# Kernel tuning notes

Measured on AMD Instinct MI355X. Metric: run time of the kernel, lower is better.

## Reference

```python
import jax, jax.numpy as jnp
import numpy as np

H = 64  # hidden size


def _lstm(hist, Wih, Whh, bih, bhh):
    # PyTorch single-layer LSTM, gate order [i, f, g, o]; hist: (T, in_dim)
    def step(carry, x):
        h, c = carry
        gates = Wih @ x + bih + Whh @ h + bhh  # (4H,)
        i, f, g, o = jnp.split(gates, 4)
        i, f, o = jax.nn.sigmoid(i), jax.nn.sigmoid(f), jax.nn.sigmoid(o)
        c = f * c + i * jnp.tanh(g)
        h = o * jnp.tanh(c)
        return (h, c), None
    h0 = jnp.zeros((H,), hist.dtype)
    (h, _), _ = jax.lax.scan(step, (h0, h0), hist)
    return h


def setup_inputs() -> dict:
    key = jax.random.key(0)
    ks = jax.random.split(key, 16)
    N, E, P, T = 100000, 3200000, 1000000, 200
    s = 0.05
    return {
        "node_feats": jax.random.normal(ks[0], (N, 2), jnp.float32),
        "edge_feats": jax.random.normal(ks[1], (E, 5), jnp.float32),
        "hist_tokens": jax.random.normal(ks[2], (T, 3), jnp.float32),
        "cand_pairs": jax.random.randint(ks[3], (P, 2), 0, N, jnp.int32),
        "N": N,
        "node_W": jax.random.normal(ks[4], (2, H), jnp.float32) * s,
        "node_b": jax.random.normal(ks[5], (H,), jnp.float32) * s,
        "edge_W": jax.random.normal(ks[6], (5, H), jnp.float32) * s,
        "edge_b": jax.random.normal(ks[7], (H,), jnp.float32) * s,
        "lstm_Wih": jax.random.normal(ks[8], (4 * H, 3), jnp.float32) * s,
        "lstm_Whh": jax.random.normal(ks[9], (4 * H, H), jnp.float32) * s,
        "lstm_bih": jax.random.normal(ks[10], (4 * H,), jnp.float32) * s,
        "lstm_bhh": jax.random.normal(ks[11], (4 * H,), jnp.float32) * s,
        "fuse_W1": jax.random.normal(ks[12], (3 * H + 2, H), jnp.float32) * s,
        "fuse_b1": jax.random.normal(ks[13], (H,), jnp.float32) * s,
        "fuse_W2": jax.random.normal(ks[14], (H, 1), jnp.float32) * s,
        "fuse_b2": jax.random.normal(ks[15], (1,), jnp.float32) * s,
    }


def reference(node_feats, edge_feats, hist_tokens, cand_pairs, N,
              node_W, node_b, edge_W, edge_b,
              lstm_Wih, lstm_Whh, lstm_bih, lstm_bhh,
              fuse_W1, fuse_b1, fuse_W2, fuse_b2):
    # encoder: mean-pooled node / edge MLPs -> (2H,)
    hn = jax.nn.relu(node_feats @ node_W + node_b).mean(0)
    he = jax.nn.relu(edge_feats @ edge_W + edge_b).mean(0)
    z_graph = jnp.concatenate([hn, he])  # (2H,)
    z_hist = _lstm(hist_tokens, lstm_Wih, lstm_Whh, lstm_bih, lstm_bhh)  # (H,)
    P = cand_pairs.shape[0]
    denom = jnp.float32(N - 1) + 1e-9
    cand = cand_pairs.astype(jnp.float32) / denom  # (P, 2)
    ctx = jnp.concatenate([z_graph, z_hist])  # (3H,)
    z = jnp.concatenate([jnp.broadcast_to(ctx, (P, 3 * H)), cand], axis=-1)  # (P, 3H+2)
    scores = jax.nn.relu(z @ fuse_W1 + fuse_b1) @ fuse_W2 + fuse_b2  # (P, 1)
    return scores[:, 0]
```

## Files before the change

kernel.cpp:

```cpp
#include <hip/hip_runtime.h>
#include <math.h>

#define H 64
#define WS_H 0
#define WS_FUSE 64
#define WS_CNT 320
#define WS_PART 384
#define LOG2E 1.4426950408889634f

__device__ __forceinline__ float fast_sigmoid(float x) {
    float e = exp2f(-LOG2E * x);
    return __builtin_amdgcn_rcpf(1.f + e);
}
__device__ __forceinline__ float fast_tanh(float x) {
    x = fminf(fmaxf(x, -9.f), 9.f);
    float e = exp2f((2.f * LOG2E) * x);
    return (e - 1.f) * __builtin_amdgcn_rcpf(e + 1.f);
}

template<int K>
__device__ void encode_rows2(const float* __restrict__ X, const float* __restrict__ Wg,
                             const float* __restrict__ bias, int nrows,
                             int blk, int nblk, float* __restrict__ out, int tid,
                             float* __restrict__ xs)
{
    constexpr int TR = 512;
    int lane = tid & 63;
    int j0 = (tid >> 6) * 16;
    float w[K][16], bi[16], acc[16];
#pragma unroll
    for (int k = 0; k < K; ++k)
#pragma unroll
        for (int jj = 0; jj < 16; ++jj) w[k][jj] = Wg[k * H + j0 + jj];
#pragma unroll
    for (int jj = 0; jj < 16; ++jj) { bi[jj] = bias[j0 + jj]; acc[jj] = 0.f; }

    int ntiles = (nrows + TR - 1) / TR;
    for (int tile = blk; tile < ntiles; tile += nblk) {
        size_t base = (size_t)tile * TR;
        int cnt = nrows - (int)base; if (cnt > TR) cnt = TR;
        int ne = cnt * K;
        __syncthreads();
        const float* Xb = X + base * K;
        int n4 = ne >> 2;
        for (int idx = tid; idx < n4; idx += 256)
            ((float4*)xs)[idx] = ((const float4*)Xb)[idx];
        for (int idx = (n4 << 2) + tid; idx < ne; idx += 256)
            xs[idx] = Xb[idx];
        __syncthreads();
#pragma unroll
        for (int i = 0; i < TR / 64; ++i) {
            int r = i * 64 + lane;
            if (r < cnt) {
                float x[K];
#pragma unroll
                for (int k = 0; k < K; ++k) x[k] = xs[r * K + k];
#pragma unroll
                for (int jj = 0; jj < 16; ++jj) {
                    float t = bi[jj];
#pragma unroll
                    for (int k = 0; k < K; ++k) t = fmaf(x[k], w[k][jj], t);
                    acc[jj] += fmaxf(t, 0.f);
                }
            }
        }
    }
#pragma unroll
    for (int jj = 0; jj < 16; ++jj) {
        float v = acc[jj];
#pragma unroll
        for (int off = 32; off; off >>= 1) v += __shfl_xor(v, off);
        if (lane == jj) out[j0 + jj] = v;
    }
}

__device__ void finalize_dev(int tid, const float* __restrict__ W1,
                             const float* __restrict__ b1, const float* __restrict__ W2,
                             float inv_n, float inv_e, float inv_denom,
                             int eb, int nb, float* __restrict__ ws, float* __restrict__ fin)
{
    float* tmpe = fin;
    float* tmpn = fin + 256;
    float* ctx  = fin + 512;
    float* pt   = fin + 704;
    int q = tid >> 6, j = tid & 63;
    const float* wsp = ws + WS_PART;

    float se = 0.f;
    for (int b = q; b < eb; b += 4) se += wsp[(size_t)b * H + j];
    tmpe[q * H + j] = se;
    float sn = 0.f;
    for (int b = q; b < nb; b += 4) sn += wsp[(size_t)(eb + b) * H + j];
    tmpn[q * H + j] = sn;
    __syncthreads();

    if (tid < H) {
        float s1 = (tmpn[tid] + tmpn[H + tid]) + (tmpn[2 * H + tid] + tmpn[3 * H + tid]);
        float s2 = (tmpe[tid] + tmpe[H + tid]) + (tmpe[2 * H + tid] + tmpe[3 * H + tid]);
        ctx[tid]         = s1 * inv_n;
        ctx[H + tid]     = s2 * inv_e;
        ctx[2 * H + tid] = ws[WS_H + tid];
    }
    __syncthreads();

    float p = 0.f;
#pragma unroll
    for (int kk = 0; kk < 48; ++kk) {
        int k = q * 48 + kk;
        p = fmaf(ctx[k], W1[(size_t)k * H + j], p);
    }
    pt[q * H + j] = p;
    __syncthreads();

    if (tid < H) {
        float bse = b1[tid] + (pt[tid] + pt[H + tid]) + (pt[2 * H + tid] + pt[3 * H + tid]);
        float4 v;
        v.x = bse;
        v.y = W1[(size_t)192 * H + tid] * inv_denom;
        v.z = W1[(size_t)193 * H + tid] * inv_denom;
        v.w = W2[tid];
        ((float4*)(ws + WS_FUSE))[tid] = v;
    }
}

__global__ __launch_bounds__(256, 2)
void k_main(const float* __restrict__ node_feats, const float* __restrict__ edge_feats,
            const float* __restrict__ hist,
            const float* __restrict__ node_W, const float* __restrict__ node_b,
            const float* __restrict__ edge_W, const float* __restrict__ edge_b,
            const float* __restrict__ Wih, const float* __restrict__ Whh,
            const float* __restrict__ bih, const float* __restrict__ bhh,
            const float* __restrict__ W1, const float* __restrict__ b1,
            const float* __restrict__ W2,
            float inv_n, float inv_e, float inv_denom,
            int Nn, int Ne, int T, int eb, int nb,
            float* __restrict__ ws)
{
    __shared__ __align__(16) char smem[12800];
    __shared__ unsigned lastflag;
    int tid = threadIdx.x;
    int b = blockIdx.x;

    if (b == 0) {
        float* pb     = (float*)smem;
        float* hist_f = (float*)(smem + 10240);
        int s = tid >> 6, j = tid & 63;
        int kbase = __builtin_amdgcn_readfirstlane((tid >> 6) << 4);

        float w[4][16];
#pragma unroll
        for (int g = 0; g < 4; ++g) {
            const float* wr = Whh + (size_t)(g * H + j) * H + kbase;
#pragma unroll
            for (int m4 = 0; m4 < 4; ++m4) {
                float4 v = *(const float4*)(wr + 4 * m4);
                w[g][4*m4+0] = v.x; w[g][4*m4+1] = v.y; w[g][4*m4+2] = v.z; w[g][4*m4+3] = v.w;
            }
        }
        float wi0[4], wi1[4], wi2[4], bb[4];
#pragma unroll
        for (int g = 0; g < 4; ++g) {
            int row = g * H + j;
            wi0[g] = Wih[row*3+0]; wi1[g] = Wih[row*3+1]; wi2[g] = Wih[row*3+2];
            bb[g] = bih[row] + bhh[row];
        }
        for (int idx = tid; idx < T * 3; idx += 256) hist_f[idx] = hist[idx];
        float hs[16];
#pragma unroll
        for (int m = 0; m < 16; ++m) hs[m] = 0.f;
        float c = 0.f, h = 0.f;
        __syncthreads();
        float x0 = hist_f[0], x1 = hist_f[1], x2 = hist_f[2];
        __builtin_amdgcn_s_setprio(1);

        for (int t = 0; t < T; ++t) {
            float a0 = 0.f, a1 = 0.f, a2 = 0.f, a3 = 0.f;
#pragma unroll
            for (int m = 0; m < 16; ++m) {
                a0 = fmaf(w[0][m], hs[m], a0);
                a1 = fmaf(w[1][m], hs[m], a1);
                a2 = fmaf(w[2][m], hs[m], a2);
                a3 = fmaf(w[3][m], hs[m], a3);
            }
            float4 part; part.x = a0; part.y = a1; part.z = a2; part.w = a3;
            *(float4*)(pb + ((size_t)((t & 1) * 64 + j)) * 20 + 4 * s) = part;
            float xb0 = fmaf(wi2[0], x2, fmaf(wi1[0], x1, fmaf(wi0[0], x0, bb[0])));
            float xb1 = fmaf(wi2[1], x2, fmaf(wi1[1], x1, fmaf(wi0[1], x0, bb[1])));
            float xb2 = fmaf(wi2[2], x2, fmaf(wi1[2], x1, fmaf(wi0[2], x0, bb[2])));
            float xb3 = fmaf(wi2[3], x2, fmaf(wi1[3], x1, fmaf(wi0[3], x0, bb[3])));
            if (t + 1 < T) { x0 = hist_f[3*t+3]; x1 = hist_f[3*t+4]; x2 = hist_f[3*t+5]; }
            __syncthreads();
            const float* row = pb + ((size_t)((t & 1) * 64 + j)) * 20;
            float4 p0 = *(const float4*)(row + 0);
            float4 p1 = *(const float4*)(row + 4);
            float4 p2 = *(const float4*)(row + 8);
            float4 p3 = *(const float4*)(row + 12);
            float gi = fast_sigmoid((p0.x + p1.x) + (p2.x + p3.x) + xb0);
            float gf = fast_sigmoid((p0.y + p1.y) + (p2.y + p3.y) + xb1);
            float gg = fast_tanh  ((p0.z + p1.z) + (p2.z + p3.z) + xb2);
            float go = fast_sigmoid((p0.w + p1.w) + (p2.w + p3.w) + xb3);
            c = fmaf(gf, c, gi * gg);
            h = go * fast_tanh(c);
#pragma unroll
            for (int m = 0; m < 16; ++m)
                hs[m] = __int_as_float(__builtin_amdgcn_readlane(__float_as_int(h), kbase + m));
        }
        __builtin_amdgcn_s_setprio(0);
        if (s == 0) ws[WS_H + j] = h;
    } else if (b <= eb) {
        encode_rows2<5>(edge_feats, edge_W, edge_b, Ne, b - 1, eb,
                        ws + WS_PART + (size_t)(b - 1) * H, tid, (float*)smem);
    } else {
        encode_rows2<2>(node_feats, node_W, node_b, Nn, b - 1 - eb, nb,
                        ws + WS_PART + (size_t)(eb + (b - 1 - eb)) * H, tid, (float*)smem);
    }

    __threadfence();
    if (tid == 0) {
        unsigned prev = atomicAdd((unsigned*)(ws + WS_CNT), 1u);
        lastflag = (prev == (unsigned)(gridDim.x - 1)) ? 1u : 0u;
    }
    __syncthreads();
    if (lastflag) {
        __threadfence();
        finalize_dev(tid, W1, b1, W2, inv_n, inv_e, inv_denom, eb, nb, ws, (float*)smem);
    }
}

__global__ __launch_bounds__(256)
void k_fuse(const int* __restrict__ pairs, const float* __restrict__ fb2,
            const float* __restrict__ ws, float* __restrict__ out, int P)
{
    __shared__ __align__(16) float4 sf[H];
    int tid = threadIdx.x;
    if (tid < H) sf[tid] = ((const float4*)(ws + WS_FUSE))[tid];
    __syncthreads();

    int i0 = blockIdx.x * 2048 + tid;
    float bias = fb2[0];
    float p0[8], p1[8], sc[8];
#pragma unroll
    for (int q = 0; q < 8; ++q) {
        int i = i0 + q * 256;
        int2 pr = (i < P) ? ((const int2*)pairs)[i] : make_int2(0, 0);
        p0[q] = (float)pr.x; p1[q] = (float)pr.y; sc[q] = bias;
    }
#pragma unroll
    for (int jj = 0; jj < H; ++jj) {
        float4 v = sf[jj];
#pragma unroll
        for (int q = 0; q < 8; ++q) {
            float hh = fmaf(p1[q], v.z, fmaf(p0[q], v.y, v.x));
            sc[q] = fmaf(fmaxf(hh, 0.f), v.w, sc[q]);
        }
    }
#pragma unroll
    for (int q = 0; q < 8; ++q) {
        int i = i0 + q * 256;
        if (i < P) out[i] = sc[q];
    }
}

extern "C" void kernel_launch(void* const* d_in, const int* in_sizes, int n_in,
                              void* d_out, int out_size, void* d_ws, size_t ws_size,
                              hipStream_t stream) {
    const float* node_feats = (const float*)d_in[0];
    const float* edge_feats = (const float*)d_in[1];
    const float* hist       = (const float*)d_in[2];
    const int*   pairs      = (const int*)d_in[3];
    const float* node_W = (const float*)d_in[5];
    const float* node_b = (const float*)d_in[6];
    const float* edge_W = (const float*)d_in[7];
    const float* edge_b = (const float*)d_in[8];
    const float* Wih    = (const float*)d_in[9];
    const float* Whh    = (const float*)d_in[10];
    const float* bih    = (const float*)d_in[11];
    const float* bhh    = (const float*)d_in[12];
    const float* W1     = (const float*)d_in[13];
    const float* b1     = (const float*)d_in[14];
    const float* W2     = (const float*)d_in[15];
    const float* b2     = (const float*)d_in[16];

    int Nn = in_sizes[0] / 2;
    int Ne = in_sizes[1] / 5;
    int T  = in_sizes[2] / 3;
    int P  = in_sizes[3] / 2;

    int eb = 448, nb = 48;
    while ((size_t)(WS_PART + (eb + nb) * H) * sizeof(float) > ws_size && eb > 8) {
        eb >>= 1; if (nb > 4) nb >>= 1;
    }

    float inv_n = (float)(1.0 / (double)Nn);
    float inv_e = (float)(1.0 / (double)Ne);
    float denomf = (float)(Nn - 1) + 1e-9f;
    float inv_denom = 1.0f / denomf;

    float* ws = (float*)d_ws;

    hipMemsetAsync((char*)d_ws + WS_CNT * sizeof(float), 0, sizeof(unsigned), stream);

    k_main<<<1 + eb + nb, 256, 0, stream>>>(
        node_feats, edge_feats, hist, node_W, node_b, edge_W, edge_b,
        Wih, Whh, bih, bhh, W1, b1, W2,
        inv_n, inv_e, inv_denom, Nn, Ne, T, eb, nb, ws);

    int blocksC = (P + 2047) / 2048;
    k_fuse<<<blocksC, 256, 0, stream>>>(pairs, b2, ws, (float*)d_out, P);
}
```

Baseline: 152.7 us.

## Split fused kernel into separate encode and single-block LSTM+finalize kernels

```diff
diff --git a/kernel.cpp b/kernel.cpp
--- a/kernel.cpp
+++ b/kernel.cpp
@@ -2,9 +2,7 @@
 #include <math.h>
 
 #define H 64
-#define WS_H 0
 #define WS_FUSE 64
-#define WS_CNT 320
 #define WS_PART 384
 #define LOG2E 1.4426950408889634f
 
@@ -74,156 +72,144 @@
     }
 }
 
-__device__ void finalize_dev(int tid, const float* __restrict__ W1,
-                             const float* __restrict__ b1, const float* __restrict__ W2,
-                             float inv_n, float inv_e, float inv_denom,
-                             int eb, int nb, float* __restrict__ ws, float* __restrict__ fin)
-{
-    float* tmpe = fin;
-    float* tmpn = fin + 256;
-    float* ctx  = fin + 512;
-    float* pt   = fin + 704;
-    int q = tid >> 6, j = tid & 63;
-    const float* wsp = ws + WS_PART;
-
-    float se = 0.f;
-    for (int b = q; b < eb; b += 4) se += wsp[(size_t)b * H + j];
-    tmpe[q * H + j] = se;
-    float sn = 0.f;
-    for (int b = q; b < nb; b += 4) sn += wsp[(size_t)(eb + b) * H + j];
-    tmpn[q * H + j] = sn;
-    __syncthreads();
-
-    if (tid < H) {
-        float s1 = (tmpn[tid] + tmpn[H + tid]) + (tmpn[2 * H + tid] + tmpn[3 * H + tid]);
-        float s2 = (tmpe[tid] + tmpe[H + tid]) + (tmpe[2 * H + tid] + tmpe[3 * H + tid]);
-        ctx[tid]         = s1 * inv_n;
-        ctx[H + tid]     = s2 * inv_e;
-        ctx[2 * H + tid] = ws[WS_H + tid];
-    }
-    __syncthreads();
-
-    float p = 0.f;
-#pragma unroll
-    for (int kk = 0; kk < 48; ++kk) {
-        int k = q * 48 + kk;
-        p = fmaf(ctx[k], W1[(size_t)k * H + j], p);
-    }
-    pt[q * H + j] = p;
-    __syncthreads();
-
-    if (tid < H) {
-        float bse = b1[tid] + (pt[tid] + pt[H + tid]) + (pt[2 * H + tid] + pt[3 * H + tid]);
-        float4 v;
-        v.x = bse;
-        v.y = W1[(size_t)192 * H + tid] * inv_denom;
-        v.z = W1[(size_t)193 * H + tid] * inv_denom;
-        v.w = W2[tid];
-        ((float4*)(ws + WS_FUSE))[tid] = v;
-    }
-}
-
 __global__ __launch_bounds__(256, 2)
-void k_main(const float* __restrict__ node_feats, const float* __restrict__ edge_feats,
-            const float* __restrict__ hist,
-            const float* __restrict__ node_W, const float* __restrict__ node_b,
-            const float* __restrict__ edge_W, const float* __restrict__ edge_b,
+void k_encode(const float* __restrict__ node_feats, const float* __restrict__ edge_feats,
+              const float* __restrict__ node_W, const float* __restrict__ node_b,
+              const float* __restrict__ edge_W, const float* __restrict__ edge_b,
+              int Nn, int Ne, int eb, int nb, float* __restrict__ ws)
+{
+    __shared__ __align__(16) float xs[2560];
+    int tid = threadIdx.x;
+    int b = blockIdx.x;
+    if (b < eb) {
+        encode_rows2<5>(edge_feats, edge_W, edge_b, Ne, b, eb,
+                        ws + WS_PART + (size_t)b * H, tid, xs);
+    } else {
+        encode_rows2<2>(node_feats, node_W, node_b, Nn, b - eb, nb,
+                        ws + WS_PART + (size_t)b * H, tid, xs);
+    }
+}
+
+__global__ __launch_bounds__(256, 2)
+void k_lstm(const float* __restrict__ hist,
             const float* __restrict__ Wih, const float* __restrict__ Whh,
             const float* __restrict__ bih, const float* __restrict__ bhh,
             const float* __restrict__ W1, const float* __restrict__ b1,
             const float* __restrict__ W2,
             float inv_n, float inv_e, float inv_denom,
-            int Nn, int Ne, int T, int eb, int nb,
-            float* __restrict__ ws)
-{
-    __shared__ __align__(16) char smem[12800];
-    __shared__ unsigned lastflag;
+            int T, int eb, int nb, float* __restrict__ ws)
+{
+    __shared__ float pbuf[2][64][17];
+    __shared__ float hist_s[608];
+    __shared__ float hsh[H];
+    __shared__ __align__(16) float fin[960];
     int tid = threadIdx.x;
-    int b = blockIdx.x;
-
-    if (b == 0) {
-        float* pb     = (float*)smem;
-        float* hist_f = (float*)(smem + 10240);
-        int s = tid >> 6, j = tid & 63;
-        int kbase = __builtin_amdgcn_readfirstlane((tid >> 6) << 4);
-
-        float w[4][16];
-#pragma unroll
-        for (int g = 0; g < 4; ++g) {
-            const float* wr = Whh + (size_t)(g * H + j) * H + kbase;
-#pragma unroll
-            for (int m4 = 0; m4 < 4; ++m4) {
-                float4 v = *(const float4*)(wr + 4 * m4);
-                w[g][4*m4+0] = v.x; w[g][4*m4+1] = v.y; w[g][4*m4+2] = v.z; w[g][4*m4+3] = v.w;
-            }
-        }
-        float wi0[4], wi1[4], wi2[4], bb[4];
-#pragma unroll
-        for (int g = 0; g < 4; ++g) {
-            int row = g * H + j;
-            wi0[g] = Wih[row*3+0]; wi1[g] = Wih[row*3+1]; wi2[g] = Wih[row*3+2];
-            bb[g] = bih[row] + bhh[row];
-        }
-        for (int idx = tid; idx < T * 3; idx += 256) hist_f[idx] = hist[idx];
-        float hs[16];
-#pragma unroll
-        for (int m = 0; m < 16; ++m) hs[m] = 0.f;
-        float c = 0.f, h = 0.f;
-        __syncthreads();
-        float x0 = hist_f[0], x1 = hist_f[1], x2 = hist_f[2];
-        __builtin_amdgcn_s_setprio(1);
-
-        for (int t = 0; t < T; ++t) {
-            float a0 = 0.f, a1 = 0.f, a2 = 0.f, a3 = 0.f;
-#pragma unroll
-            for (int m = 0; m < 16; ++m) {
-                a0 = fmaf(w[0][m], hs[m], a0);
-                a1 = fmaf(w[1][m], hs[m], a1);
-                a2 = fmaf(w[2][m], hs[m], a2);
-                a3 = fmaf(w[3][m], hs[m], a3);
-            }
-            float4 part; part.x = a0; part.y = a1; part.z = a2; part.w = a3;
-            *(float4*)(pb + ((size_t)((t & 1) * 64 + j)) * 20 + 4 * s) = part;
-            float xb0 = fmaf(wi2[0], x2, fmaf(wi1[0], x1, fmaf(wi0[0], x0, bb[0])));
-            float xb1 = fmaf(wi2[1], x2, fmaf(wi1[1], x1, fmaf(wi0[1], x0, bb[1])));
-            float xb2 = fmaf(wi2[2], x2, fmaf(wi1[2], x1, fmaf(wi0[2], x0, bb[2])));
-            float xb3 = fmaf(wi2[3], x2, fmaf(wi1[3], x1, fmaf(wi0[3], x0, bb[3])));
-            if (t + 1 < T) { x0 = hist_f[3*t+3]; x1 = hist_f[3*t+4]; x2 = hist_f[3*t+5]; }
-            __syncthreads();
-            const float* row = pb + ((size_t)((t & 1) * 64 + j)) * 20;
-            float4 p0 = *(const float4*)(row + 0);
-            float4 p1 = *(const float4*)(row + 4);
-            float4 p2 = *(const float4*)(row + 8);
-            float4 p3 = *(const float4*)(row + 12);
-            float gi = fast_sigmoid((p0.x + p1.x) + (p2.x + p3.x) + xb0);
-            float gf = fast_sigmoid((p0.y + p1.y) + (p2.y + p3.y) + xb1);
-            float gg = fast_tanh  ((p0.z + p1.z) + (p2.z + p3.z) + xb2);
-            float go = fast_sigmoid((p0.w + p1.w) + (p2.w + p3.w) + xb3);
-            c = fmaf(gf, c, gi * gg);
-            h = go * fast_tanh(c);
-#pragma unroll
-            for (int m = 0; m < 16; ++m)
-                hs[m] = __int_as_float(__builtin_amdgcn_readlane(__float_as_int(h), kbase + m));
-        }
-        __builtin_amdgcn_s_setprio(0);
-        if (s == 0) ws[WS_H + j] = h;
-    } else if (b <= eb) {
-        encode_rows2<5>(edge_feats, edge_W, edge_b, Ne, b - 1, eb,
-                        ws + WS_PART + (size_t)(b - 1) * H, tid, (float*)smem);
-    } else {
-        encode_rows2<2>(node_feats, node_W, node_b, Nn, b - 1 - eb, nb,
-                        ws + WS_PART + (size_t)(eb + (b - 1 - eb)) * H, tid, (float*)smem);
-    }
-
-    __threadfence();
-    if (tid == 0) {
-        unsigned prev = atomicAdd((unsigned*)(ws + WS_CNT), 1u);
-        lastflag = (prev == (unsigned)(gridDim.x - 1)) ? 1u : 0u;
-    }
+    int s = tid >> 6, j = tid & 63;
+    int kb = __builtin_amdgcn_readfirstlane((tid >> 6) << 4);
+
+    float w[4][16];
+#pragma unroll
+    for (int g = 0; g < 4; ++g) {
+        const float* wr = Whh + (size_t)(g * H + j) * H + kb;
+#pragma unroll
+        for (int m4 = 0; m4 < 4; ++m4) {
+            float4 v = *(const float4*)(wr + 4 * m4);
+            w[g][4*m4+0] = v.x; w[g][4*m4+1] = v.y; w[g][4*m4+2] = v.z; w[g][4*m4+3] = v.w;
+        }
+    }
+    float wi0[4], wi1[4], wi2[4], bb[4];
+#pragma unroll
+    for (int g = 0; g < 4; ++g) {
+        int row = g * H + j;
+        wi0[g] = Wih[row*3+0]; wi1[g] = Wih[row*3+1]; wi2[g] = Wih[row*3+2];
+        bb[g] = bih[row] + bhh[row];
+    }
+    for (int idx = tid; idx < T * 3; idx += 256) hist_s[idx] = hist[idx];
+    float hs[16];
+#pragma unroll
+    for (int m = 0; m < 16; ++m) hs[m] = 0.f;
+    float c = 0.f, h = 0.f;
     __syncthreads();
-    if (lastflag) {
-        __threadfence();
-        finalize_dev(tid, W1, b1, W2, inv_n, inv_e, inv_denom, eb, nb, ws, (float*)smem);
+    float x0 = hist_s[0], x1 = hist_s[1], x2 = hist_s[2];
+
+    for (int t = 0; t < T; ++t) {
+        int p = t & 1;
+        float a0 = 0.f, a1 = 0.f, a2 = 0.f, a3 = 0.f;
+#pragma unroll
+        for (int m = 0; m < 16; ++m) {
+            a0 = fmaf(w[0][m], hs[m], a0);
+            a1 = fmaf(w[1][m], hs[m], a1);
+            a2 = fmaf(w[2][m], hs[m], a2);
+            a3 = fmaf(w[3][m], hs[m], a3);
+        }
+        float* prow = &pbuf[p][j][4 * s];
+        prow[0] = a0; prow[1] = a1; prow[2] = a2; prow[3] = a3;
+        float xb0 = fmaf(wi2[0], x2, fmaf(wi1[0], x1, fmaf(wi0[0], x0, bb[0])));
+        float xb1 = fmaf(wi2[1], x2, fmaf(wi1[1], x1, fmaf(wi0[1], x0, bb[1])));
+        float xb2 = fmaf(wi2[2], x2, fmaf(wi1[2], x1, fmaf(wi0[2], x0, bb[2])));
+        float xb3 = fmaf(wi2[3], x2, fmaf(wi1[3], x1, fmaf(wi0[3], x0, bb[3])));
+        if (t + 1 < T) { x0 = hist_s[3*t+3]; x1 = hist_s[3*t+4]; x2 = hist_s[3*t+5]; }
+        __syncthreads();
+        const float* rrow = pbuf[p][j];
+        float q0 = rrow[0], q1 = rrow[1], q2 = rrow[2],  q3 = rrow[3];
+        float q4 = rrow[4], q5 = rrow[5], q6 = rrow[6],  q7 = rrow[7];
+        float q8 = rrow[8], q9 = rrow[9], qa = rrow[10], qb = rrow[11];
+        float qc = rrow[12], qd = rrow[13], qe = rrow[14], qf = rrow[15];
+        float gi = fast_sigmoid(((q0 + q4) + (q8 + qc)) + xb0);
+        float gf = fast_sigmoid(((q1 + q5) + (q9 + qd)) + xb1);
+        float gg = fast_tanh  (((q2 + q6) + (qa + qe)) + xb2);
+        float go = fast_sigmoid(((q3 + q7) + (qb + qf)) + xb3);
+        c = fmaf(gf, c, gi * gg);
+        h = go * fast_tanh(c);
+#pragma unroll
+        for (int m = 0; m < 16; ++m)
+            hs[m] = __int_as_float(__builtin_amdgcn_readlane(__float_as_int(h), kb + m));
+    }
+    if (s == 0) hsh[j] = h;
+    __syncthreads();
+
+    {
+        float* tmpe = fin;
+        float* tmpn = fin + 256;
+        float* ctx  = fin + 512;
+        float* pt   = fin + 704;
+        const float* wsp = ws + WS_PART;
+
+        float se = 0.f;
+        for (int b = s; b < eb; b += 4) se += wsp[(size_t)b * H + j];
+        tmpe[s * H + j] = se;
+        float sn = 0.f;
+        for (int b = s; b < nb; b += 4) sn += wsp[(size_t)(eb + b) * H + j];
+        tmpn[s * H + j] = sn;
+        __syncthreads();
+
+        if (tid < H) {
+            float s1 = (tmpn[tid] + tmpn[H + tid]) + (tmpn[2 * H + tid] + tmpn[3 * H + tid]);
+            float s2 = (tmpe[tid] + tmpe[H + tid]) + (tmpe[2 * H + tid] + tmpe[3 * H + tid]);
+            ctx[tid]         = s1 * inv_n;
+            ctx[H + tid]     = s2 * inv_e;
+            ctx[2 * H + tid] = hsh[tid];
+        }
+        __syncthreads();
+
+        float p = 0.f;
+#pragma unroll
+        for (int kk = 0; kk < 48; ++kk) {
+            int k = s * 48 + kk;
+            p = fmaf(ctx[k], W1[(size_t)k * H + j], p);
+        }
+        pt[s * H + j] = p;
+        __syncthreads();
+
+        if (tid < H) {
+            float bse = b1[tid] + (pt[tid] + pt[H + tid]) + (pt[2 * H + tid] + pt[3 * H + tid]);
+            float4 v;
+            v.x = bse;
+            v.y = W1[(size_t)192 * H + tid] * inv_denom;
+            v.z = W1[(size_t)193 * H + tid] * inv_denom;
+            v.w = W2[tid];
+            ((float4*)(ws + WS_FUSE))[tid] = v;
+        }
     }
 }
 
@@ -286,7 +272,7 @@
     int T  = in_sizes[2] / 3;
     int P  = in_sizes[3] / 2;
 
-    int eb = 448, nb = 48;
+    int eb = 1024, nb = 64;
     while ((size_t)(WS_PART + (eb + nb) * H) * sizeof(float) > ws_size && eb > 8) {
         eb >>= 1; if (nb > 4) nb >>= 1;
     }
@@ -298,12 +284,13 @@
 
     float* ws = (float*)d_ws;
 
-    hipMemsetAsync((char*)d_ws + WS_CNT * sizeof(float), 0, sizeof(unsigned), stream);
-
-    k_main<<<1 + eb + nb, 256, 0, stream>>>(
-        node_feats, edge_feats, hist, node_W, node_b, edge_W, edge_b,
-        Wih, Whh, bih, bhh, W1, b1, W2,
-        inv_n, inv_e, inv_denom, Nn, Ne, T, eb, nb, ws);
+    k_encode<<<eb + nb, 256, 0, stream>>>(
+        node_feats, edge_feats, node_W, node_b, edge_W, edge_b,
+        Nn, Ne, eb, nb, ws);
+
+    k_lstm<<<1, 256, 0, stream>>>(
+        hist, Wih, Whh, bih, bhh, W1, b1, W2,
+        inv_n, inv_e, inv_denom, T, eb, nb, ws);
 
     int blocksC = (P + 2047) / 2048;
     k_fuse<<<blocksC, 256, 0, stream>>>(pairs, b2, ws, (float*)d_out, P);
```

Result: slower. 235.6 us (+54.3%).

## Widen main kernel to 512 threads and split LSTM and encoder work finer

Applied to the files above, without the earlier changes.

```diff
diff --git a/kernel.cpp b/kernel.cpp
--- a/kernel.cpp
+++ b/kernel.cpp
@@ -17,113 +17,120 @@
     float e = exp2f((2.f * LOG2E) * x);
     return (e - 1.f) * __builtin_amdgcn_rcpf(e + 1.f);
 }
-
-template<int K>
-__device__ void encode_rows2(const float* __restrict__ X, const float* __restrict__ Wg,
-                             const float* __restrict__ bias, int nrows,
-                             int blk, int nblk, float* __restrict__ out, int tid,
-                             float* __restrict__ xs)
+__device__ __forceinline__ float4 f4fma(float s, float4 a, float4 b) {
+    b.x = fmaf(s, a.x, b.x); b.y = fmaf(s, a.y, b.y);
+    b.z = fmaf(s, a.z, b.z); b.w = fmaf(s, a.w, b.w); return b;
+}
+__device__ __forceinline__ float4 f4add(float4 a, float4 b) {
+    a.x += b.x; a.y += b.y; a.z += b.z; a.w += b.w; return a;
+}
+__device__ __forceinline__ float4 f4reluacc(float4 t, float4 a) {
+    a.x += fmaxf(t.x, 0.f); a.y += fmaxf(t.y, 0.f);
+    a.z += fmaxf(t.z, 0.f); a.w += fmaxf(t.w, 0.f); return a;
+}
+#define WREDUCE(x) { x += __shfl_xor(x, 1); x += __shfl_xor(x, 2); x += __shfl_xor(x, 4); \
+                     x += __shfl_xor(x, 8); x += __shfl_xor(x, 16); x += __shfl_xor(x, 32); }
+
+__device__ void encode_edge(const float* __restrict__ X, const float* __restrict__ Wg,
+                            const float* __restrict__ bias, int nrows,
+                            int blk, int nblk, float* __restrict__ out, float* __restrict__ xs)
 {
-    constexpr int TR = 512;
-    int lane = tid & 63;
-    int j0 = (tid >> 6) * 16;
-    float w[K][16], bi[16], acc[16];
-#pragma unroll
-    for (int k = 0; k < K; ++k)
-#pragma unroll
-        for (int jj = 0; jj < 16; ++jj) w[k][jj] = Wg[k * H + j0 + jj];
-#pragma unroll
-    for (int jj = 0; jj < 16; ++jj) { bi[jj] = bias[j0 + jj]; acc[jj] = 0.f; }
-
-    int ntiles = (nrows + TR - 1) / TR;
+    int tid = threadIdx.x, lane = tid & 63, s = tid >> 6;
+    int j0 = s * 8;
+    float4 wa0 = *(const float4*)(Wg + 0*H + j0), wb0 = *(const float4*)(Wg + 0*H + j0 + 4);
+    float4 wa1 = *(const float4*)(Wg + 1*H + j0), wb1 = *(const float4*)(Wg + 1*H + j0 + 4);
+    float4 wa2 = *(const float4*)(Wg + 2*H + j0), wb2 = *(const float4*)(Wg + 2*H + j0 + 4);
+    float4 wa3 = *(const float4*)(Wg + 3*H + j0), wb3 = *(const float4*)(Wg + 3*H + j0 + 4);
+    float4 wa4 = *(const float4*)(Wg + 4*H + j0), wb4 = *(const float4*)(Wg + 4*H + j0 + 4);
+    float4 bia = *(const float4*)(bias + j0),     bib = *(const float4*)(bias + j0 + 4);
+    float4 acca = {0.f,0.f,0.f,0.f}, accb = {0.f,0.f,0.f,0.f};
+
+    int ntiles = (nrows + 255) >> 8;
     for (int tile = blk; tile < ntiles; tile += nblk) {
-        size_t base = (size_t)tile * TR;
-        int cnt = nrows - (int)base; if (cnt > TR) cnt = TR;
-        int ne = cnt * K;
-        __syncthreads();
-        const float* Xb = X + base * K;
-        int n4 = ne >> 2;
-        for (int idx = tid; idx < n4; idx += 256)
-            ((float4*)xs)[idx] = ((const float4*)Xb)[idx];
-        for (int idx = (n4 << 2) + tid; idx < ne; idx += 256)
-            xs[idx] = Xb[idx];
-        __syncthreads();
-#pragma unroll
-        for (int i = 0; i < TR / 64; ++i) {
-            int r = i * 64 + lane;
+        long base = (long)tile << 8;
+        int rem = (int)(nrows - base);
+        int cnt = rem > 256 ? 256 : rem;
+        int nw = cnt * 5;
+        __syncthreads();
+        const float* Xb = X + base * 5;
+        int n4 = nw >> 2;
+        for (int idx = tid; idx < n4; idx += 512) ((float4*)xs)[idx] = ((const float4*)Xb)[idx];
+        for (int idx = (n4 << 2) + tid; idx < nw; idx += 512) xs[idx] = Xb[idx];
+        __syncthreads();
+#pragma unroll
+        for (int ri = 0; ri < 4; ++ri) {
+            int r = ri * 64 + lane;
             if (r < cnt) {
-                float x[K];
-#pragma unroll
-                for (int k = 0; k < K; ++k) x[k] = xs[r * K + k];
-#pragma unroll
-                for (int jj = 0; jj < 16; ++jj) {
-                    float t = bi[jj];
-#pragma unroll
-                    for (int k = 0; k < K; ++k) t = fmaf(x[k], w[k][jj], t);
-                    acc[jj] += fmaxf(t, 0.f);
-                }
+                float x0 = xs[r*5+0], x1 = xs[r*5+1], x2 = xs[r*5+2], x3 = xs[r*5+3], x4 = xs[r*5+4];
+                float4 ta = bia, tb = bib;
+                ta = f4fma(x0, wa0, ta); tb = f4fma(x0, wb0, tb);
+                ta = f4fma(x1, wa1, ta); tb = f4fma(x1, wb1, tb);
+                ta = f4fma(x2, wa2, ta); tb = f4fma(x2, wb2, tb);
+                ta = f4fma(x3, wa3, ta); tb = f4fma(x3, wb3, tb);
+                ta = f4fma(x4, wa4, ta); tb = f4fma(x4, wb4, tb);
+                acca = f4reluacc(ta, acca); accb = f4reluacc(tb, accb);
             }
         }
     }
-#pragma unroll
-    for (int jj = 0; jj < 16; ++jj) {
-        float v = acc[jj];
-#pragma unroll
-        for (int off = 32; off; off >>= 1) v += __shfl_xor(v, off);
-        if (lane == jj) out[j0 + jj] = v;
-    }
-}
-
-__device__ void finalize_dev(int tid, const float* __restrict__ W1,
-                             const float* __restrict__ b1, const float* __restrict__ W2,
-                             float inv_n, float inv_e, float inv_denom,
-                             int eb, int nb, float* __restrict__ ws, float* __restrict__ fin)
+    WREDUCE(acca.x) WREDUCE(acca.y) WREDUCE(acca.z) WREDUCE(acca.w)
+    WREDUCE(accb.x) WREDUCE(accb.y) WREDUCE(accb.z) WREDUCE(accb.w)
+    if (lane == 0) {
+        *(float4*)(out + j0) = acca;
+        *(float4*)(out + j0 + 4) = accb;
+    }
+}
+
+__device__ void encode_node(const float* __restrict__ X, const float* __restrict__ Wg,
+                            const float* __restrict__ bias, int nrows,
+                            int blk, int nblk, float* __restrict__ out, float* __restrict__ xs)
 {
-    float* tmpe = fin;
-    float* tmpn = fin + 256;
-    float* ctx  = fin + 512;
-    float* pt   = fin + 704;
-    int q = tid >> 6, j = tid & 63;
-    const float* wsp = ws + WS_PART;
-
-    float se = 0.f;
-    for (int b = q; b < eb; b += 4) se += wsp[(size_t)b * H + j];
-    tmpe[q * H + j] = se;
-    float sn = 0.f;
-    for (int b = q; b < nb; b += 4) sn += wsp[(size_t)(eb + b) * H + j];
-    tmpn[q * H + j] = sn;
-    __syncthreads();
-
-    if (tid < H) {
-        float s1 = (tmpn[tid] + tmpn[H + tid]) + (tmpn[2 * H + tid] + tmpn[3 * H + tid]);
-        float s2 = (tmpe[tid] + tmpe[H + tid]) + (tmpe[2 * H + tid] + tmpe[3 * H + tid]);
-        ctx[tid]         = s1 * inv_n;
-        ctx[H + tid]     = s2 * inv_e;
-        ctx[2 * H + tid] = ws[WS_H + tid];
-    }
-    __syncthreads();
-
-    float p = 0.f;
-#pragma unroll
-    for (int kk = 0; kk < 48; ++kk) {
-        int k = q * 48 + kk;
-        p = fmaf(ctx[k], W1[(size_t)k * H + j], p);
-    }
-    pt[q * H + j] = p;
-    __syncthreads();
-
-    if (tid < H) {
-        float bse = b1[tid] + (pt[tid] + pt[H + tid]) + (pt[2 * H + tid] + pt[3 * H + tid]);
-        float4 v;
-        v.x = bse;
-        v.y = W1[(size_t)192 * H + tid] * inv_denom;
-        v.z = W1[(size_t)193 * H + tid] * inv_denom;
-        v.w = W2[tid];
-        ((float4*)(ws + WS_FUSE))[tid] = v;
-    }
-}
-
-__global__ __launch_bounds__(256, 2)
+    int tid = threadIdx.x, lane = tid & 63, s = tid >> 6;
+    int j0 = s * 8;
+    float4 wa0 = *(const float4*)(Wg + 0*H + j0), wb0 = *(const float4*)(Wg + 0*H + j0 + 4);
+    float4 wa1 = *(const float4*)(Wg + 1*H + j0), wb1 = *(const float4*)(Wg + 1*H + j0 + 4);
+    float4 bia = *(const float4*)(bias + j0),     bib = *(const float4*)(bias + j0 + 4);
+    float4 acca = {0.f,0.f,0.f,0.f}, accb = {0.f,0.f,0.f,0.f};
+
+    int ntiles = (nrows + 255) >> 8;
+    for (int tile = blk; tile < ntiles; tile += nblk) {
+        long base = (long)tile << 8;
+        int rem = (int)(nrows - base);
+        int cnt = rem > 256 ? 256 : rem;
+        int nw = cnt * 2;
+        __syncthreads();
+        const float* Xb = X + base * 2;
+        int n4 = nw >> 2;
+        for (int idx = tid; idx < n4; idx += 512) ((float4*)xs)[idx] = ((const float4*)Xb)[idx];
+        for (int idx = (n4 << 2) + tid; idx < nw; idx += 512) xs[idx] = Xb[idx];
+        __syncthreads();
+#pragma unroll
+        for (int ri = 0; ri < 4; ++ri) {
+            int r = ri * 64 + lane;
+            if (r < cnt) {
+                float x0 = xs[r*2+0], x1 = xs[r*2+1];
+                float4 ta = bia, tb = bib;
+                ta = f4fma(x0, wa0, ta); tb = f4fma(x0, wb0, tb);
+                ta = f4fma(x1, wa1, ta); tb = f4fma(x1, wb1, tb);
+                acca = f4reluacc(ta, acca); accb = f4reluacc(tb, accb);
+            }
+        }
+    }
+    WREDUCE(acca.x) WREDUCE(acca.y) WREDUCE(acca.z) WREDUCE(acca.w)
+    WREDUCE(accb.x) WREDUCE(accb.y) WREDUCE(accb.z) WREDUCE(accb.w)
+    if (lane == 0) {
+        *(float4*)(out + j0) = acca;
+        *(float4*)(out + j0 + 4) = accb;
+    }
+}
+
+#define GATE_DOT(res, wA, wB) do { float _t = 0.f; \
+    _t = fmaf((wA).x, hsA.x, _t); _t = fmaf((wA).y, hsA.y, _t); \
+    _t = fmaf((wA).z, hsA.z, _t); _t = fmaf((wA).w, hsA.w, _t); \
+    _t = fmaf((wB).x, hsB.x, _t); _t = fmaf((wB).y, hsB.y, _t); \
+    _t = fmaf((wB).z, hsB.z, _t); _t = fmaf((wB).w, hsB.w, _t); \
+    res = _t; } while (0)
+
+__global__ __launch_bounds__(512)
 void k_main(const float* __restrict__ node_feats, const float* __restrict__ edge_feats,
             const float* __restrict__ hist,
             const float* __restrict__ node_W, const float* __restrict__ node_b,
@@ -136,83 +143,91 @@
             int Nn, int Ne, int T, int eb, int nb,
             float* __restrict__ ws)
 {
-    __shared__ __align__(16) char smem[12800];
+    __shared__ __align__(16) char smem[22912];
     __shared__ unsigned lastflag;
     int tid = threadIdx.x;
     int b = blockIdx.x;
 
     if (b == 0) {
-        float* pb     = (float*)smem;
-        float* hist_f = (float*)(smem + 10240);
-        int s = tid >> 6, j = tid & 63;
-        int kbase = __builtin_amdgcn_readfirstlane((tid >> 6) << 4);
-
-        float w[4][16];
-#pragma unroll
-        for (int g = 0; g < 4; ++g) {
-            const float* wr = Whh + (size_t)(g * H + j) * H + kbase;
-#pragma unroll
-            for (int m4 = 0; m4 < 4; ++m4) {
-                float4 v = *(const float4*)(wr + 4 * m4);
-                w[g][4*m4+0] = v.x; w[g][4*m4+1] = v.y; w[g][4*m4+2] = v.z; w[g][4*m4+3] = v.w;
-            }
-        }
-        float wi0[4], wi1[4], wi2[4], bb[4];
-#pragma unroll
-        for (int g = 0; g < 4; ++g) {
-            int row = g * H + j;
-            wi0[g] = Wih[row*3+0]; wi1[g] = Wih[row*3+1]; wi2[g] = Wih[row*3+2];
-            bb[g] = bih[row] + bhh[row];
-        }
-        for (int idx = tid; idx < T * 3; idx += 256) hist_f[idx] = hist[idx];
-        float hs[16];
-#pragma unroll
-        for (int m = 0; m < 16; ++m) hs[m] = 0.f;
+        float* pbuf   = (float*)smem;
+        float* hist_s = (float*)(smem + 16384);
+        float4* wib   = (float4*)(smem + 18816);
+        int j = tid & 63, s = tid >> 6;
+        int kb = __builtin_amdgcn_readfirstlane(s << 3);
+        int swz = j & 7;
+
+        float4 w0a = *(const float4*)(Whh + (size_t)(0*H + j)*H + kb);
+        float4 w0b = *(const float4*)(Whh + (size_t)(0*H + j)*H + kb + 4);
+        float4 w1a = *(const float4*)(Whh + (size_t)(1*H + j)*H + kb);
+        float4 w1b = *(const float4*)(Whh + (size_t)(1*H + j)*H + kb + 4);
+        float4 w2a = *(const float4*)(Whh + (size_t)(2*H + j)*H + kb);
+        float4 w2b = *(const float4*)(Whh + (size_t)(2*H + j)*H + kb + 4);
+        float4 w3a = *(const float4*)(Whh + (size_t)(3*H + j)*H + kb);
+        float4 w3b = *(const float4*)(Whh + (size_t)(3*H + j)*H + kb + 4);
+
+        if (tid < 256) {
+            float4 v;
+            v.x = Wih[tid*3+0]; v.y = Wih[tid*3+1]; v.z = Wih[tid*3+2];
+            v.w = bih[tid] + bhh[tid];
+            wib[tid] = v;
+        }
+        for (int idx = tid; idx < T * 3; idx += 512) hist_s[idx] = hist[idx];
+        float4 hsA = {0.f,0.f,0.f,0.f}, hsB = {0.f,0.f,0.f,0.f};
         float c = 0.f, h = 0.f;
         __syncthreads();
-        float x0 = hist_f[0], x1 = hist_f[1], x2 = hist_f[2];
+        float x0 = hist_s[0], x1 = hist_s[1], x2 = hist_s[2];
         __builtin_amdgcn_s_setprio(1);
 
         for (int t = 0; t < T; ++t) {
-            float a0 = 0.f, a1 = 0.f, a2 = 0.f, a3 = 0.f;
-#pragma unroll
-            for (int m = 0; m < 16; ++m) {
-                a0 = fmaf(w[0][m], hs[m], a0);
-                a1 = fmaf(w[1][m], hs[m], a1);
-                a2 = fmaf(w[2][m], hs[m], a2);
-                a3 = fmaf(w[3][m], hs[m], a3);
-            }
-            float4 part; part.x = a0; part.y = a1; part.z = a2; part.w = a3;
-            *(float4*)(pb + ((size_t)((t & 1) * 64 + j)) * 20 + 4 * s) = part;
-            float xb0 = fmaf(wi2[0], x2, fmaf(wi1[0], x1, fmaf(wi0[0], x0, bb[0])));
-            float xb1 = fmaf(wi2[1], x2, fmaf(wi1[1], x1, fmaf(wi0[1], x0, bb[1])));
-            float xb2 = fmaf(wi2[2], x2, fmaf(wi1[2], x1, fmaf(wi0[2], x0, bb[2])));
-            float xb3 = fmaf(wi2[3], x2, fmaf(wi1[3], x1, fmaf(wi0[3], x0, bb[3])));
-            if (t + 1 < T) { x0 = hist_f[3*t+3]; x1 = hist_f[3*t+4]; x2 = hist_f[3*t+5]; }
+            float* pb = pbuf + ((t & 1) << 11) + (j << 5);
+            float a0, a1, a2, a3;
+            GATE_DOT(a0, w0a, w0b);
+            GATE_DOT(a1, w1a, w1b);
+            GATE_DOT(a2, w2a, w2b);
+            GATE_DOT(a3, w3a, w3b);
+            float4 pq; pq.x = a0; pq.y = a1; pq.z = a2; pq.w = a3;
+            *(float4*)(pb + ((s ^ swz) << 2)) = pq;
+            float4 v0 = wib[j], v1 = wib[64 + j], v2 = wib[128 + j], v3 = wib[192 + j];
+            float xb0 = fmaf(v0.z, x2, fmaf(v0.y, x1, fmaf(v0.x, x0, v0.w)));
+            float xb1 = fmaf(v1.z, x2, fmaf(v1.y, x1, fmaf(v1.x, x0, v1.w)));
+            float xb2 = fmaf(v2.z, x2, fmaf(v2.y, x1, fmaf(v2.x, x0, v2.w)));
+            float xb3 = fmaf(v3.z, x2, fmaf(v3.y, x1, fmaf(v3.x, x0, v3.w)));
+            if (t + 1 < T) { x0 = hist_s[3*t+3]; x1 = hist_s[3*t+4]; x2 = hist_s[3*t+5]; }
             __syncthreads();
-            const float* row = pb + ((size_t)((t & 1) * 64 + j)) * 20;
-            float4 p0 = *(const float4*)(row + 0);
-            float4 p1 = *(const float4*)(row + 4);
-            float4 p2 = *(const float4*)(row + 8);
-            float4 p3 = *(const float4*)(row + 12);
-            float gi = fast_sigmoid((p0.x + p1.x) + (p2.x + p3.x) + xb0);
-            float gf = fast_sigmoid((p0.y + p1.y) + (p2.y + p3.y) + xb1);
-            float gg = fast_tanh  ((p0.z + p1.z) + (p2.z + p3.z) + xb2);
-            float go = fast_sigmoid((p0.w + p1.w) + (p2.w + p3.w) + xb3);
+            float4 r0 = *(const float4*)(pb + ((0 ^ swz) << 2));
+            float4 r1 = *(const float4*)(pb + ((1 ^ swz) << 2));
+            float4 r2 = *(const float4*)(pb + ((2 ^ swz) << 2));
+            float4 r3 = *(const float4*)(pb + ((3 ^ swz) << 2));
+            float4 r4 = *(const float4*)(pb + ((4 ^ swz) << 2));
+            float4 r5 = *(const float4*)(pb + ((5 ^ swz) << 2));
+            float4 r6 = *(const float4*)(pb + ((6 ^ swz) << 2));
+            float4 r7 = *(const float4*)(pb + ((7 ^ swz) << 2));
+            float4 sum = f4add(f4add(f4add(r0, r1), f4add(r2, r3)),
+                               f4add(f4add(r4, r5), f4add(r6, r7)));
+            float gi = fast_sigmoid(sum.x + xb0);
+            float gf = fast_sigmoid(sum.y + xb1);
+            float gg = fast_tanh  (sum.z + xb2);
+            float go = fast_sigmoid(sum.w + xb3);
             c = fmaf(gf, c, gi * gg);
             h = go * fast_tanh(c);
-#pragma unroll
-            for (int m = 0; m < 16; ++m)
-                hs[m] = __int_as_float(__builtin_amdgcn_readlane(__float_as_int(h), kbase + m));
+            int hi = __float_as_int(h);
+            hsA.x = __int_as_float(__builtin_amdgcn_readlane(hi, kb + 0));
+            hsA.y = __int_as_float(__builtin_amdgcn_readlane(hi, kb + 1));
+            hsA.z = __int_as_float(__builtin_amdgcn_readlane(hi, kb + 2));
+            hsA.w = __int_as_float(__builtin_amdgcn_readlane(hi, kb + 3));
+            hsB.x = __int_as_float(__builtin_amdgcn_readlane(hi, kb + 4));
+            hsB.y = __int_as_float(__builtin_amdgcn_readlane(hi, kb + 5));
+            hsB.z = __int_as_float(__builtin_amdgcn_readlane(hi, kb + 6));
+            hsB.w = __int_as_float(__builtin_amdgcn_readlane(hi, kb + 7));
         }
         __builtin_amdgcn_s_setprio(0);
         if (s == 0) ws[WS_H + j] = h;
     } else if (b <= eb) {
-        encode_rows2<5>(edge_feats, edge_W, edge_b, Ne, b - 1, eb,
-                        ws + WS_PART + (size_t)(b - 1) * H, tid, (float*)smem);
+        encode_edge(edge_feats, edge_W, edge_b, Ne, b - 1, eb,
+                    ws + WS_PART + (size_t)(b - 1) * H, (float*)smem);
     } else {
-        encode_rows2<2>(node_feats, node_W, node_b, Nn, b - 1 - eb, nb,
-                        ws + WS_PART + (size_t)(eb + (b - 1 - eb)) * H, tid, (float*)smem);
+        encode_node(node_feats, node_W, node_b, Nn, b - 1 - eb, nb,
+                    ws + WS_PART + (size_t)(b - 1) * H, (float*)smem);
     }
 
     __threadfence();
@@ -223,7 +238,52 @@
     __syncthreads();
     if (lastflag) {
         __threadfence();
-        finalize_dev(tid, W1, b1, W2, inv_n, inv_e, inv_denom, eb, nb, ws, (float*)smem);
+        float* fin  = (float*)smem;
+        float* tmpe = fin;
+        float* tmpn = fin + 512;
+        float* ctx  = fin + 1024;
+        float* pt   = fin + 1216;
+        int q = tid >> 6, j = tid & 63;
+        const float* wsp = ws + WS_PART;
+
+        float se = 0.f;
+        for (int bb = q; bb < eb; bb += 8) se += wsp[(size_t)bb * H + j];
+        tmpe[q * H + j] = se;
+        float sn = 0.f;
+        for (int bb = q; bb < nb; bb += 8) sn += wsp[(size_t)(eb + bb) * H + j];
+        tmpn[q * H + j] = sn;
+        __syncthreads();
+
+        if (tid < H) {
+            float s1 = 0.f, s2 = 0.f;
+#pragma unroll
+            for (int r = 0; r < 8; ++r) { s1 += tmpn[r * H + tid]; s2 += tmpe[r * H + tid]; }
+            ctx[tid]         = s1 * inv_n;
+            ctx[H + tid]     = s2 * inv_e;
+            ctx[2 * H + tid] = ws[WS_H + tid];
+        }
+        __syncthreads();
+
+        float p = 0.f;
+#pragma unroll
+        for (int kk = 0; kk < 24; ++kk) {
+            int k = q * 24 + kk;
+            p = fmaf(ctx[k], W1[(size_t)k * H + j], p);
+        }
+        pt[q * H + j] = p;
+        __syncthreads();
+
+        if (tid < H) {
+            float bse = b1[tid];
+#pragma unroll
+            for (int r = 0; r < 8; ++r) bse += pt[r * H + tid];
+            float4 v;
+            v.x = bse;
+            v.y = W1[(size_t)192 * H + tid] * inv_denom;
+            v.z = W1[(size_t)193 * H + tid] * inv_denom;
+            v.w = W2[tid];
+            ((float4*)(ws + WS_FUSE))[tid] = v;
+        }
     }
 }
 
@@ -286,7 +346,7 @@
     int T  = in_sizes[2] / 3;
     int P  = in_sizes[3] / 2;
 
-    int eb = 448, nb = 48;
+    int eb = 960, nb = 63;
     while ((size_t)(WS_PART + (eb + nb) * H) * sizeof(float) > ws_size && eb > 8) {
         eb >>= 1; if (nb > 4) nb >>= 1;
     }
@@ -300,7 +360,7 @@
 
     hipMemsetAsync((char*)d_ws + WS_CNT * sizeof(float), 0, sizeof(unsigned), stream);
 
-    k_main<<<1 + eb + nb, 256, 0, stream>>>(
+    k_main<<<1 + eb + nb, 512, 0, stream>>>(
         node_feats, edge_feats, hist, node_W, node_b, edge_W, edge_b,
         Wih, Whh, bih, bhh, W1, b1, W2,
         inv_n, inv_e, inv_denom, Nn, Ne, T, eb, nb, ws);
```

After: 237.6 us. 1.56x slower.
